# Kernel tuning notes

Hardware: AMD Instinct MI355X
Metric: run time of the kernel (lower is better)

Reference implementation:

```python
import jax, jax.numpy as jnp
import numpy as np

N = 50000
E = 1600000
D_IN = 128
HID = 128
EPS = 1e-5
NEG_SLOPE = 0.2


def setup_inputs() -> dict:
    key = jax.random.key(0)
    ks = jax.random.split(key, 16)
    s = 1.0 / np.sqrt(D_IN)
    inp = {
        'x': jax.random.normal(ks[0], (N, D_IN), dtype=jnp.float32),
        'edge_index': jax.random.randint(ks[1], (2, E), 0, N, dtype=jnp.int64),
        # layer 0 params
        'W0': jax.random.normal(ks[2], (D_IN, HID), dtype=jnp.float32) * s,
        'att_src0': jax.random.normal(ks[3], (HID,), dtype=jnp.float32) * s,
        'att_dst0': jax.random.normal(ks[4], (HID,), dtype=jnp.float32) * s,
        'bias0': jnp.zeros((HID,), dtype=jnp.float32),
        'gamma0': jnp.ones((HID,), dtype=jnp.float32),
        'beta0': jnp.zeros((HID,), dtype=jnp.float32),
        # layer 1 params
        'W1': jax.random.normal(ks[5], (HID, HID), dtype=jnp.float32) * s,
        'att_src1': jax.random.normal(ks[6], (HID,), dtype=jnp.float32) * s,
        'att_dst1': jax.random.normal(ks[7], (HID,), dtype=jnp.float32) * s,
        'bias1': jnp.zeros((HID,), dtype=jnp.float32),
        'gamma1': jnp.ones((HID,), dtype=jnp.float32),
        'beta1': jnp.zeros((HID,), dtype=jnp.float32),
    }
    return inp


def _gat_conv(x, W, a_src, a_dst, bias, src, dst, n_nodes):
    h = x @ W                                   # [N, HID]
    alpha_src = h @ a_src                       # [N]
    alpha_dst = h @ a_dst                       # [N]
    e = jax.nn.leaky_relu(alpha_src[src] + alpha_dst[dst], NEG_SLOPE)  # [E']
    # numerically stable softmax over edges grouped by destination node
    m = jax.ops.segment_max(e, dst, num_segments=n_nodes)
    ex = jnp.exp(e - m[dst])
    denom = jax.ops.segment_sum(ex, dst, num_segments=n_nodes)
    alpha = ex / denom[dst]                     # [E']
    out = jax.ops.segment_sum(h[src] * alpha[:, None], dst, num_segments=n_nodes)
    return out + bias


def _batch_norm(x, gamma, beta):
    mean = jnp.mean(x, axis=0)
    var = jnp.mean(jnp.square(x - mean), axis=0)  # biased variance (torch BN normalization)
    return gamma * (x - mean) * jax.lax.rsqrt(var + EPS) + beta


def reference(x, edge_index, W0, att_src0, att_dst0, bias0, gamma0, beta0,
              W1, att_src1, att_dst1, bias1, gamma1, beta1):
    n = x.shape[0]
    loops = jnp.arange(n, dtype=edge_index.dtype)
    src = jnp.concatenate([edge_index[0], loops])
    dst = jnp.concatenate([edge_index[1], loops])

    h = _gat_conv(x, W0, att_src0, att_dst0, bias0, src, dst, n)
    h = _batch_norm(h, gamma0, beta0)
    h = jax.nn.relu(h)
    # dropout: identity in eval mode

    h = _gat_conv(h, W1, att_src1, att_dst1, bias1, src, dst, n)
    h = _batch_norm(h, gamma1, beta1)
    h = jax.nn.relu(h)  # last_activation=True
    return h
```

## Files before the change

kernel.cpp:

```cpp
#include <hip/hip_runtime.h>
#include <math.h>

#define HID 128
#define PAD 96
#define NB 196
#define CAP 10240
#define CHUNK 4096
#define AGG_BLOCKS 2048
#define NEG_SLOPE 0.2f
#define EPS 1e-5f

static __device__ __forceinline__ unsigned bf16_rne(float x) {
    unsigned u = __float_as_uint(x);
    return (u + 0x7fffu + ((u >> 16) & 1u)) >> 16;
}
static __device__ __forceinline__ unsigned pack_bf16(float lo, float hi) {
    return bf16_rne(lo) | (bf16_rne(hi) << 16);
}

template <bool BN>
__global__ __launch_bounds__(256) void gemm_alpha(
    const float* __restrict__ X, const float* __restrict__ W,
    const float* __restrict__ a_src, const float* __restrict__ a_dst,
    const float* __restrict__ coef,
    unsigned* __restrict__ Hb, float* __restrict__ asrc, float* __restrict__ adst,
    int N)
{
    __shared__ float Ws[HID * HID];
    int tid = threadIdx.x;
#pragma unroll
    for (int i = 0; i < 16; ++i) {
        int idx = tid * 4 + i * 1024;
        *(float4*)&Ws[idx] = *(const float4*)&W[idx];
    }
    __syncthreads();

    int tx = tid & 15, ty = tid >> 4;
    int row0 = blockIdx.x * 128 + ty * 8;
    int c0 = tx * 8;

    const float* xr[8];
    bool valid[8];
#pragma unroll
    for (int r = 0; r < 8; ++r) {
        int row = row0 + r;
        valid[r] = (row < N);
        xr[r] = X + (size_t)(valid[r] ? row : 0) * HID;
    }

    float acc[8][8];
#pragma unroll
    for (int r = 0; r < 8; ++r)
#pragma unroll
        for (int c = 0; c < 8; ++c) acc[r][c] = 0.f;

    for (int kb = 0; kb < HID / 4; ++kb) {
        float4 sc4, sh4;
        if (BN) {
            sc4 = *(const float4*)&coef[kb * 4];
            sh4 = *(const float4*)&coef[HID + kb * 4];
        }
        float4 xv[8];
#pragma unroll
        for (int r = 0; r < 8; ++r) {
            xv[r] = *(const float4*)(xr[r] + kb * 4);
            if (BN) {
                xv[r].x = fmaxf(fmaf(xv[r].x, sc4.x, sh4.x), 0.f);
                xv[r].y = fmaxf(fmaf(xv[r].y, sc4.y, sh4.y), 0.f);
                xv[r].z = fmaxf(fmaf(xv[r].z, sc4.z, sh4.z), 0.f);
                xv[r].w = fmaxf(fmaf(xv[r].w, sc4.w, sh4.w), 0.f);
            }
        }
#pragma unroll
        for (int kk = 0; kk < 4; ++kk) {
            float4 w0 = *(const float4*)&Ws[(kb * 4 + kk) * HID + c0];
            float4 w1 = *(const float4*)&Ws[(kb * 4 + kk) * HID + c0 + 4];
#pragma unroll
            for (int r = 0; r < 8; ++r) {
                float xk = (&xv[r].x)[kk];
                acc[r][0] = fmaf(xk, w0.x, acc[r][0]);
                acc[r][1] = fmaf(xk, w0.y, acc[r][1]);
                acc[r][2] = fmaf(xk, w0.z, acc[r][2]);
                acc[r][3] = fmaf(xk, w0.w, acc[r][3]);
                acc[r][4] = fmaf(xk, w1.x, acc[r][4]);
                acc[r][5] = fmaf(xk, w1.y, acc[r][5]);
                acc[r][6] = fmaf(xk, w1.z, acc[r][6]);
                acc[r][7] = fmaf(xk, w1.w, acc[r][7]);
            }
        }
    }

    float4 asv0 = *(const float4*)&a_src[c0];
    float4 asv1 = *(const float4*)&a_src[c0 + 4];
    float4 adv0 = *(const float4*)&a_dst[c0];
    float4 adv1 = *(const float4*)&a_dst[c0 + 4];

#pragma unroll
    for (int r = 0; r < 8; ++r) {
        float s = acc[r][0] * asv0.x + acc[r][1] * asv0.y + acc[r][2] * asv0.z +
                  acc[r][3] * asv0.w + acc[r][4] * asv1.x + acc[r][5] * asv1.y +
                  acc[r][6] * asv1.z + acc[r][7] * asv1.w;
        float d = acc[r][0] * adv0.x + acc[r][1] * adv0.y + acc[r][2] * adv0.z +
                  acc[r][3] * adv0.w + acc[r][4] * adv1.x + acc[r][5] * adv1.y +
                  acc[r][6] * adv1.z + acc[r][7] * adv1.w;
#pragma unroll
        for (int o = 1; o < 16; o <<= 1) {
            s += __shfl_xor(s, o);
            d += __shfl_xor(d, o);
        }
        if (tx == 0 && valid[r]) { asrc[row0 + r] = s; adst[row0 + r] = d; }
        if (valid[r]) {
            uint4 st;
            st.x = pack_bf16(acc[r][0], acc[r][1]);
            st.y = pack_bf16(acc[r][2], acc[r][3]);
            st.z = pack_bf16(acc[r][4], acc[r][5]);
            st.w = pack_bf16(acc[r][6], acc[r][7]);
            *(uint4*)&Hb[(size_t)(row0 + r) * 64 + (c0 >> 1)] = st;
        }
    }
}

__global__ __launch_bounds__(256) void scatter_part(
    const int* __restrict__ ei, int* __restrict__ bcur,
    unsigned int* __restrict__ bbuf, int E)
{
    __shared__ int lcnt[NB], gbase[NB];
    int tid = threadIdx.x;
    int i0 = blockIdx.x * CHUNK;
    int i1 = i0 + CHUNK; if (i1 > E) i1 = E;
    if (tid < NB) lcnt[tid] = 0;
    __syncthreads();
    for (int i = i0 + tid; i < i1; i += 256)
        atomicAdd(&lcnt[ei[E + i] >> 8], 1);
    __syncthreads();
    if (tid < NB) {
        gbase[tid] = atomicAdd(&bcur[tid], lcnt[tid]);
        lcnt[tid] = 0;
    }
    __syncthreads();
    for (int i = i0 + tid; i < i1; i += 256) {
        int s = ei[i], d = ei[E + i];
        int b = d >> 8;
        int off = atomicAdd(&lcnt[b], 1);
        int pos = gbase[b] + off;
        if (pos < CAP)
            bbuf[(size_t)b * CAP + pos] = ((unsigned)s << 8) | (unsigned)(d & 255);
    }
}

__global__ __launch_bounds__(256) void ell_build(
    const unsigned int* __restrict__ bbuf, const int* __restrict__ bcur,
    int* __restrict__ cnt, int* __restrict__ ell, int N)
{
    __shared__ int stage[256 * PAD];
    __shared__ int scnt[256];
    int tid = threadIdx.x;
    int b = blockIdx.x;
    int base = b << 8;
    int nodes = N - base; if (nodes > 256) nodes = 256;

    for (int i = tid; i < nodes; i += 256) {
        stage[i * PAD] = base + i;
        scnt[i] = 1;
    }
    __syncthreads();

    int nb = bcur[b]; if (nb > CAP) nb = CAP;
    const unsigned int* buf = bbuf + (size_t)b * CAP;
    for (int j = tid; j < nb; j += 256) {
        unsigned int v = buf[j];
        int dl = (int)(v & 255u);
        int s = (int)(v >> 8);
        int p = atomicAdd(&scnt[dl], 1);
        if (p < PAD) stage[dl * PAD + p] = s;
    }
    __syncthreads();

    int total = nodes * PAD;
    int* dst = ell + (size_t)base * PAD;
    for (int idx = tid * 4; idx < total; idx += 1024)
        *(int4*)&dst[idx] = *(const int4*)&stage[idx];
    for (int i = tid; i < nodes; i += 256)
        cnt[base + i] = scnt[i];
}

__global__ __launch_bounds__(256) void gat_aggregate(
    const unsigned* __restrict__ Hb, const float* __restrict__ asrc,
    const float* __restrict__ adst, const int* __restrict__ cnt,
    const int* __restrict__ ell, const float* __restrict__ bias,
    float* __restrict__ OUT, float* __restrict__ stat, int N)
{
    __shared__ float sbuf[4][HID], qbuf[4][HID];
    int tid = threadIdx.x, wave = tid >> 6, lane = tid & 63;
    int c0 = 2 * lane;
    float b0 = bias[c0], b1 = bias[c0 + 1];
    float ssum0 = 0.f, ssum1 = 0.f, sq0 = 0.f, sq1 = 0.f;

    for (int n = blockIdx.x * 4 + wave; n < N; n += AGG_BLOCKS * 4) {
        int nn = __builtin_amdgcn_readfirstlane(n);
        int deg = cnt[nn];
        if (deg > PAD) deg = PAD;
        const int* row = ell + (size_t)nn * PAD;
        float adn = adst[nn];

        float acc0 = 0.f, acc1 = 0.f, den = 0.f;
#define EDGE(SI) { int si = (SI);                                   \
        float v = asrc[si] + adn;                                   \
        v = v > 0.f ? v : NEG_SLOPE * v;                            \
        float w = __expf(v);                                        \
        den += w;                                                   \
        unsigned hv = Hb[(size_t)si * 64 + lane];                   \
        acc0 = fmaf(w, __uint_as_float(hv << 16), acc0);            \
        acc1 = fmaf(w, __uint_as_float(hv & 0xffff0000u), acc1); }
        int j = 0;
        for (; j + 4 <= deg; j += 4) {
            int4 s4 = *(const int4*)&row[j];
            EDGE(s4.x) EDGE(s4.y) EDGE(s4.z) EDGE(s4.w)
        }
        for (; j < deg; ++j) EDGE(row[j])
#undef EDGE
        float inv = 1.f / den;
        float o0 = fmaf(acc0, inv, b0);
        float o1 = fmaf(acc1, inv, b1);
        *(float2*)&OUT[(size_t)nn * HID + c0] = make_float2(o0, o1);
        ssum0 += o0; ssum1 += o1;
        sq0 = fmaf(o0, o0, sq0); sq1 = fmaf(o1, o1, sq1);
    }

    sbuf[wave][c0] = ssum0; sbuf[wave][c0 + 1] = ssum1;
    qbuf[wave][c0] = sq0;   qbuf[wave][c0 + 1] = sq1;
    __syncthreads();
    if (tid < HID) {
        float t = sbuf[0][tid] + sbuf[1][tid] + sbuf[2][tid] + sbuf[3][tid];
        atomicAdd(&stat[tid], t);
    } else {
        int c = tid - HID;
        float t = qbuf[0][c] + qbuf[1][c] + qbuf[2][c] + qbuf[3][c];
        atomicAdd(&stat[HID + c], t);
    }
}

__global__ void bn_coef(const float* __restrict__ stat, const float* __restrict__ gamma,
                        const float* __restrict__ beta, float* __restrict__ coef,
                        float invN)
{
    int c = threadIdx.x;
    float mean = stat[c] * invN;
    float var = stat[HID + c] * invN - mean * mean;
    float s = gamma[c] * rsqrtf(var + EPS);
    coef[c] = s;
    coef[HID + c] = beta[c] - mean * s;
}

__global__ __launch_bounds__(256) void bn_apply(
    float* __restrict__ X, const float* __restrict__ coef, int N)
{
    int tid = threadIdx.x, lane = tid & 63, wave = tid >> 6;
    int c0 = 2 * lane;
    float s0 = coef[c0], s1 = coef[c0 + 1];
    float h0 = coef[HID + c0], h1 = coef[HID + c0 + 1];
    for (int r = blockIdx.x * 4 + wave; r < N; r += gridDim.x * 4) {
        float2 v = *(float2*)&X[(size_t)r * HID + c0];
        float y0 = fmaxf(fmaf(v.x, s0, h0), 0.f);
        float y1 = fmaxf(fmaf(v.y, s1, h1), 0.f);
        *(float2*)&X[(size_t)r * HID + c0] = make_float2(y0, y1);
    }
}

extern "C" void kernel_launch(void* const* d_in, const int* in_sizes, int n_in,
                              void* d_out, int out_size, void* d_ws, size_t ws_size,
                              hipStream_t stream)
{
    const float* x        = (const float*)d_in[0];
    const int*   ei       = (const int*)d_in[1];
    const float* W0       = (const float*)d_in[2];
    const float* att_src0 = (const float*)d_in[3];
    const float* att_dst0 = (const float*)d_in[4];
    const float* bias0    = (const float*)d_in[5];
    const float* gamma0   = (const float*)d_in[6];
    const float* beta0    = (const float*)d_in[7];
    const float* W1       = (const float*)d_in[8];
    const float* att_src1 = (const float*)d_in[9];
    const float* att_dst1 = (const float*)d_in[10];
    const float* bias1    = (const float*)d_in[11];
    const float* gamma1   = (const float*)d_in[12];
    const float* beta1    = (const float*)d_in[13];

    const int N = in_sizes[0] / HID;
    const int E = in_sizes[1] / 2;
    float* out = (float*)d_out;

    char* wsbase = (char*)d_ws;
    size_t off = 0;
    auto alloc = [&](size_t bytes) -> void* {
        void* p = wsbase + off;
        off += (bytes + 255) & ~(size_t)255;
        return p;
    };
    unsigned*     Hb    = (unsigned*)alloc((size_t)N * HID * 2);
    float*        asrc  = (float*)alloc((size_t)N * 4);
    float*        adst  = (float*)alloc((size_t)N * 4);
    int*          cnt   = (int*)  alloc((size_t)N * 4);
    int*          ell   = (int*)  alloc((size_t)N * PAD * 4);
    unsigned int* bbuf  = (unsigned int*)alloc((size_t)NB * CAP * 4);
    int*          bcur  = (int*)  alloc(NB * 4);
    float*        stats = (float*)alloc(4 * HID * 4);
    float*        coef0 = (float*)alloc(2 * HID * 4);
    float*        coef1 = (float*)alloc(2 * HID * 4);
    float* stat0 = stats;
    float* stat1 = stats + 2 * HID;

    const int gemm_blocks = (N + 127) / 128;
    const int part_blocks = (E + CHUNK - 1) / CHUNK;
    const int build_blocks = (N + 255) / 256;
    const float invN = 1.0f / (float)N;

    (void)hipMemsetAsync(bcur, 0, NB * 4, stream);
    (void)hipMemsetAsync(stats, 0, 4 * HID * 4, stream);

    scatter_part<<<part_blocks, 256, 0, stream>>>(ei, bcur, bbuf, E);
    ell_build<<<build_blocks, 256, 0, stream>>>(bbuf, bcur, cnt, ell, N);

    gemm_alpha<false><<<gemm_blocks, 256, 0, stream>>>(
        x, W0, att_src0, att_dst0, nullptr, Hb, asrc, adst, N);
    gat_aggregate<<<AGG_BLOCKS, 256, 0, stream>>>(
        Hb, asrc, adst, cnt, ell, bias0, out, stat0, N);
    bn_coef<<<1, HID, 0, stream>>>(stat0, gamma0, beta0, coef0, invN);

    gemm_alpha<true><<<gemm_blocks, 256, 0, stream>>>(
        out, W1, att_src1, att_dst1, coef0, Hb, asrc, adst, N);
    gat_aggregate<<<AGG_BLOCKS, 256, 0, stream>>>(
        Hb, asrc, adst, cnt, ell, bias1, out, stat1, N);
    bn_coef<<<1, HID, 0, stream>>>(stat1, gamma1, beta1, coef1, invN);
    bn_apply<<<2048, 256, 0, stream>>>(out, coef1, N);
}
```

Measured before the change: 325.7 us.

## Use bf16 MFMA for feature GEMM and half-wave-per-node aggregation

Replaces the FP32 register-tiled GEMM with bf16 MFMA 16x16x32 instructions, reading a transposed bf16 copy of each weight matrix that a small kernel builds at the start. The aggregation kernel now gives each half-wave one node and each lane four channels, loading edges in groups of eight with masking, and zero-fills the ELL staging so the padded slots are safe to read. This is meant to cut GEMM compute time and raise memory-level parallelism in the gather. In exchange, the input activations are also rounded to bf16, which adds precision loss, and the gather does some wasted work on padded edges.

New measurement: 338.3 us. 3.9% more time.

```diff
diff --git a/kernel.cpp b/kernel.cpp
--- a/kernel.cpp
+++ b/kernel.cpp
@@ -10,112 +10,114 @@
 #define NEG_SLOPE 0.2f
 #define EPS 1e-5f
 
+typedef __attribute__((ext_vector_type(8))) short short8;
+typedef __attribute__((ext_vector_type(4))) float floatx4;
+
 static __device__ __forceinline__ unsigned bf16_rne(float x) {
     unsigned u = __float_as_uint(x);
     return (u + 0x7fffu + ((u >> 16) & 1u)) >> 16;
 }
-static __device__ __forceinline__ unsigned pack_bf16(float lo, float hi) {
-    return bf16_rne(lo) | (bf16_rne(hi) << 16);
+static __device__ __forceinline__ float bf16lo_f(unsigned u) { return __uint_as_float(u << 16); }
+static __device__ __forceinline__ float bf16hi_f(unsigned u) { return __uint_as_float(u & 0xffff0000u); }
+
+__global__ void wt_build(const float* __restrict__ W, unsigned short* __restrict__ Wt) {
+    int t = threadIdx.x;
+    for (int task = t; task < 2048; task += 256) {
+        int c = task & 127, k0 = (task >> 7) * 8;
+        unsigned v[8];
+#pragma unroll
+        for (int j = 0; j < 8; ++j) v[j] = bf16_rne(W[(k0 + j) * HID + c]);
+        uint4 st;
+        st.x = v[0] | (v[1] << 16);
+        st.y = v[2] | (v[3] << 16);
+        st.z = v[4] | (v[5] << 16);
+        st.w = v[6] | (v[7] << 16);
+        *(uint4*)&Wt[c * HID + k0] = st;
+    }
 }
 
 template <bool BN>
-__global__ __launch_bounds__(256) void gemm_alpha(
-    const float* __restrict__ X, const float* __restrict__ W,
+__global__ __launch_bounds__(256) void gemm_mfma(
+    const float* __restrict__ X, const unsigned short* __restrict__ Wt,
     const float* __restrict__ a_src, const float* __restrict__ a_dst,
     const float* __restrict__ coef,
-    unsigned* __restrict__ Hb, float* __restrict__ asrc, float* __restrict__ adst,
+    unsigned short* __restrict__ Hb, float* __restrict__ asrc, float* __restrict__ adst,
     int N)
 {
-    __shared__ float Ws[HID * HID];
     int tid = threadIdx.x;
-#pragma unroll
-    for (int i = 0; i < 16; ++i) {
-        int idx = tid * 4 + i * 1024;
-        *(float4*)&Ws[idx] = *(const float4*)&W[idx];
-    }
-    __syncthreads();
-
-    int tx = tid & 15, ty = tid >> 4;
-    int row0 = blockIdx.x * 128 + ty * 8;
-    int c0 = tx * 8;
-
-    const float* xr[8];
-    bool valid[8];
-#pragma unroll
-    for (int r = 0; r < 8; ++r) {
-        int row = row0 + r;
-        valid[r] = (row < N);
-        xr[r] = X + (size_t)(valid[r] ? row : 0) * HID;
-    }
-
-    float acc[8][8];
-#pragma unroll
-    for (int r = 0; r < 8; ++r)
-#pragma unroll
-        for (int c = 0; c < 8; ++c) acc[r][c] = 0.f;
-
-    for (int kb = 0; kb < HID / 4; ++kb) {
-        float4 sc4, sh4;
+    int wv = tid >> 6, lane = tid & 63;
+    int g = lane >> 4, c = lane & 15;
+    int r0w = blockIdx.x * 64 + wv * 16;
+    int arow = r0w + c;
+    bool avalid = arow < N;
+    const float* xr = X + (size_t)(avalid ? arow : 0) * HID;
+
+    floatx4 acc[8];
+#pragma unroll
+    for (int i = 0; i < 8; ++i) acc[i] = (floatx4)0.f;
+
+#pragma unroll
+    for (int kc = 0; kc < 4; ++kc) {
+        int k0 = kc * 32 + g * 8;
+        float xv[8];
+        float4 x0 = *(const float4*)&xr[k0];
+        float4 x1 = *(const float4*)&xr[k0 + 4];
+        xv[0] = x0.x; xv[1] = x0.y; xv[2] = x0.z; xv[3] = x0.w;
+        xv[4] = x1.x; xv[5] = x1.y; xv[6] = x1.z; xv[7] = x1.w;
         if (BN) {
-            sc4 = *(const float4*)&coef[kb * 4];
-            sh4 = *(const float4*)&coef[HID + kb * 4];
-        }
-        float4 xv[8];
-#pragma unroll
-        for (int r = 0; r < 8; ++r) {
-            xv[r] = *(const float4*)(xr[r] + kb * 4);
-            if (BN) {
-                xv[r].x = fmaxf(fmaf(xv[r].x, sc4.x, sh4.x), 0.f);
-                xv[r].y = fmaxf(fmaf(xv[r].y, sc4.y, sh4.y), 0.f);
-                xv[r].z = fmaxf(fmaf(xv[r].z, sc4.z, sh4.z), 0.f);
-                xv[r].w = fmaxf(fmaf(xv[r].w, sc4.w, sh4.w), 0.f);
-            }
-        }
-#pragma unroll
-        for (int kk = 0; kk < 4; ++kk) {
-            float4 w0 = *(const float4*)&Ws[(kb * 4 + kk) * HID + c0];
-            float4 w1 = *(const float4*)&Ws[(kb * 4 + kk) * HID + c0 + 4];
-#pragma unroll
-            for (int r = 0; r < 8; ++r) {
-                float xk = (&xv[r].x)[kk];
-                acc[r][0] = fmaf(xk, w0.x, acc[r][0]);
-                acc[r][1] = fmaf(xk, w0.y, acc[r][1]);
-                acc[r][2] = fmaf(xk, w0.z, acc[r][2]);
-                acc[r][3] = fmaf(xk, w0.w, acc[r][3]);
-                acc[r][4] = fmaf(xk, w1.x, acc[r][4]);
-                acc[r][5] = fmaf(xk, w1.y, acc[r][5]);
-                acc[r][6] = fmaf(xk, w1.z, acc[r][6]);
-                acc[r][7] = fmaf(xk, w1.w, acc[r][7]);
-            }
-        }
-    }
-
-    float4 asv0 = *(const float4*)&a_src[c0];
-    float4 asv1 = *(const float4*)&a_src[c0 + 4];
-    float4 adv0 = *(const float4*)&a_dst[c0];
-    float4 adv1 = *(const float4*)&a_dst[c0 + 4];
-
-#pragma unroll
-    for (int r = 0; r < 8; ++r) {
-        float s = acc[r][0] * asv0.x + acc[r][1] * asv0.y + acc[r][2] * asv0.z +
-                  acc[r][3] * asv0.w + acc[r][4] * asv1.x + acc[r][5] * asv1.y +
-                  acc[r][6] * asv1.z + acc[r][7] * asv1.w;
-        float d = acc[r][0] * adv0.x + acc[r][1] * adv0.y + acc[r][2] * adv0.z +
-                  acc[r][3] * adv0.w + acc[r][4] * adv1.x + acc[r][5] * adv1.y +
-                  acc[r][6] * adv1.z + acc[r][7] * adv1.w;
+            float4 s0 = *(const float4*)&coef[k0];
+            float4 s1 = *(const float4*)&coef[k0 + 4];
+            float4 h0 = *(const float4*)&coef[HID + k0];
+            float4 h1 = *(const float4*)&coef[HID + k0 + 4];
+            xv[0] = fmaxf(fmaf(xv[0], s0.x, h0.x), 0.f);
+            xv[1] = fmaxf(fmaf(xv[1], s0.y, h0.y), 0.f);
+            xv[2] = fmaxf(fmaf(xv[2], s0.z, h0.z), 0.f);
+            xv[3] = fmaxf(fmaf(xv[3], s0.w, h0.w), 0.f);
+            xv[4] = fmaxf(fmaf(xv[4], s1.x, h1.x), 0.f);
+            xv[5] = fmaxf(fmaf(xv[5], s1.y, h1.y), 0.f);
+            xv[6] = fmaxf(fmaf(xv[6], s1.z, h1.z), 0.f);
+            xv[7] = fmaxf(fmaf(xv[7], s1.w, h1.w), 0.f);
+        }
+        short8 af;
+#pragma unroll
+        for (int j = 0; j < 8; ++j) af[j] = avalid ? (short)bf16_rne(xv[j]) : (short)0;
+
+#pragma unroll
+        for (int nt = 0; nt < 8; ++nt) {
+            short8 bf = *(const short8*)&Wt[(nt * 16 + c) * HID + k0];
+            acc[nt] = __builtin_amdgcn_mfma_f32_16x16x32_bf16(af, bf, acc[nt], 0, 0, 0);
+        }
+    }
+
+    float as_c[8], ad_c[8];
+#pragma unroll
+    for (int nt = 0; nt < 8; ++nt) {
+        as_c[nt] = a_src[nt * 16 + c];
+        ad_c[nt] = a_dst[nt * 16 + c];
+    }
+#pragma unroll
+    for (int reg = 0; reg < 4; ++reg) {
+        float s = 0.f, d = 0.f;
+#pragma unroll
+        for (int nt = 0; nt < 8; ++nt) {
+            s = fmaf(acc[nt][reg], as_c[nt], s);
+            d = fmaf(acc[nt][reg], ad_c[nt], d);
+        }
 #pragma unroll
         for (int o = 1; o < 16; o <<= 1) {
             s += __shfl_xor(s, o);
             d += __shfl_xor(d, o);
         }
-        if (tx == 0 && valid[r]) { asrc[row0 + r] = s; adst[row0 + r] = d; }
-        if (valid[r]) {
-            uint4 st;
-            st.x = pack_bf16(acc[r][0], acc[r][1]);
-            st.y = pack_bf16(acc[r][2], acc[r][3]);
-            st.z = pack_bf16(acc[r][4], acc[r][5]);
-            st.w = pack_bf16(acc[r][6], acc[r][7]);
-            *(uint4*)&Hb[(size_t)(row0 + r) * 64 + (c0 >> 1)] = st;
+        int crow = r0w + g * 4 + reg;
+        if (c == 0 && crow < N) { asrc[crow] = s; adst[crow] = d; }
+    }
+#pragma unroll
+    for (int reg = 0; reg < 4; ++reg) {
+        int crow = r0w + g * 4 + reg;
+        if (crow < N) {
+#pragma unroll
+            for (int nt = 0; nt < 8; ++nt)
+                Hb[(size_t)crow * HID + nt * 16 + c] = (unsigned short)bf16_rne(acc[nt][reg]);
         }
     }
 }
@@ -159,6 +161,10 @@
     int base = b << 8;
     int nodes = N - base; if (nodes > 256) nodes = 256;
 
+    int4 z4; z4.x = z4.y = z4.z = z4.w = 0;
+    for (int idx = tid * 4; idx < 256 * PAD; idx += 1024)
+        *(int4*)&stage[idx] = z4;
+    __syncthreads();
     for (int i = tid; i < nodes; i += 256) {
         stage[i * PAD] = base + i;
         scnt[i] = 1;
@@ -185,58 +191,72 @@
 }
 
 __global__ __launch_bounds__(256) void gat_aggregate(
-    const unsigned* __restrict__ Hb, const float* __restrict__ asrc,
+    const unsigned short* __restrict__ Hb, const float* __restrict__ asrc,
     const float* __restrict__ adst, const int* __restrict__ cnt,
     const int* __restrict__ ell, const float* __restrict__ bias,
     float* __restrict__ OUT, float* __restrict__ stat, int N)
 {
     __shared__ float sbuf[4][HID], qbuf[4][HID];
-    int tid = threadIdx.x, wave = tid >> 6, lane = tid & 63;
-    int c0 = 2 * lane;
-    float b0 = bias[c0], b1 = bias[c0 + 1];
-    float ssum0 = 0.f, ssum1 = 0.f, sq0 = 0.f, sq1 = 0.f;
-
-    for (int n = blockIdx.x * 4 + wave; n < N; n += AGG_BLOCKS * 4) {
-        int nn = __builtin_amdgcn_readfirstlane(n);
-        int deg = cnt[nn];
-        if (deg > PAD) deg = PAD;
-        const int* row = ell + (size_t)nn * PAD;
-        float adn = adst[nn];
-
-        float acc0 = 0.f, acc1 = 0.f, den = 0.f;
-#define EDGE(SI) { int si = (SI);                                   \
-        float v = asrc[si] + adn;                                   \
-        v = v > 0.f ? v : NEG_SLOPE * v;                            \
-        float w = __expf(v);                                        \
-        den += w;                                                   \
-        unsigned hv = Hb[(size_t)si * 64 + lane];                   \
-        acc0 = fmaf(w, __uint_as_float(hv << 16), acc0);            \
-        acc1 = fmaf(w, __uint_as_float(hv & 0xffff0000u), acc1); }
-        int j = 0;
-        for (; j + 4 <= deg; j += 4) {
-            int4 s4 = *(const int4*)&row[j];
-            EDGE(s4.x) EDGE(s4.y) EDGE(s4.z) EDGE(s4.w)
-        }
-        for (; j < deg; ++j) EDGE(row[j])
-#undef EDGE
+    int tid = threadIdx.x, wv = tid >> 6, lane = tid & 63;
+    int half = lane >> 5, li = lane & 31;
+    int c0 = 4 * li;
+    float4 b4 = *(const float4*)&bias[c0];
+    float s0 = 0.f, s1 = 0.f, s2 = 0.f, s3 = 0.f;
+    float q0 = 0.f, q1 = 0.f, q2 = 0.f, q3 = 0.f;
+
+    for (int n = blockIdx.x * 8 + wv * 2 + half; n < N; n += AGG_BLOCKS * 8) {
+        int deg = cnt[n]; if (deg > PAD) deg = PAD;
+        const int* row = ell + (size_t)n * PAD;
+        float adn = adst[n];
+        float a0 = 0.f, a1 = 0.f, a2 = 0.f, a3 = 0.f, den = 0.f;
+
+        for (int j = 0; j < deg; j += 8) {
+            int4 sA = *(const int4*)&row[j];
+            int4 sB = *(const int4*)&row[j + 4];
+#define EDG(SI, JOFF) { int si = (SI);                                \
+            float v = asrc[si] + adn;                                 \
+            v = fmaxf(v, 0.f) + NEG_SLOPE * fminf(v, 0.f);            \
+            float w = ((j + JOFF) < deg) ? __expf(v) : 0.f;           \
+            den += w;                                                 \
+            uint2 hv = *(const uint2*)&Hb[(size_t)si * HID + c0];     \
+            a0 = fmaf(w, bf16lo_f(hv.x), a0);                         \
+            a1 = fmaf(w, bf16hi_f(hv.x), a1);                         \
+            a2 = fmaf(w, bf16lo_f(hv.y), a2);                         \
+            a3 = fmaf(w, bf16hi_f(hv.y), a3); }
+            EDG(sA.x, 0) EDG(sA.y, 1) EDG(sA.z, 2) EDG(sA.w, 3)
+            EDG(sB.x, 4) EDG(sB.y, 5) EDG(sB.z, 6) EDG(sB.w, 7)
+#undef EDG
+        }
         float inv = 1.f / den;
-        float o0 = fmaf(acc0, inv, b0);
-        float o1 = fmaf(acc1, inv, b1);
-        *(float2*)&OUT[(size_t)nn * HID + c0] = make_float2(o0, o1);
-        ssum0 += o0; ssum1 += o1;
-        sq0 = fmaf(o0, o0, sq0); sq1 = fmaf(o1, o1, sq1);
-    }
-
-    sbuf[wave][c0] = ssum0; sbuf[wave][c0 + 1] = ssum1;
-    qbuf[wave][c0] = sq0;   qbuf[wave][c0 + 1] = sq1;
+        float4 o;
+        o.x = fmaf(a0, inv, b4.x);
+        o.y = fmaf(a1, inv, b4.y);
+        o.z = fmaf(a2, inv, b4.z);
+        o.w = fmaf(a3, inv, b4.w);
+        *(float4*)&OUT[(size_t)n * HID + c0] = o;
+        s0 += o.x; s1 += o.y; s2 += o.z; s3 += o.w;
+        q0 = fmaf(o.x, o.x, q0); q1 = fmaf(o.y, o.y, q1);
+        q2 = fmaf(o.z, o.z, q2); q3 = fmaf(o.w, o.w, q3);
+    }
+
+    s0 += __shfl_xor(s0, 32); s1 += __shfl_xor(s1, 32);
+    s2 += __shfl_xor(s2, 32); s3 += __shfl_xor(s3, 32);
+    q0 += __shfl_xor(q0, 32); q1 += __shfl_xor(q1, 32);
+    q2 += __shfl_xor(q2, 32); q3 += __shfl_xor(q3, 32);
+    if (half == 0) {
+        sbuf[wv][c0] = s0; sbuf[wv][c0 + 1] = s1;
+        sbuf[wv][c0 + 2] = s2; sbuf[wv][c0 + 3] = s3;
+        qbuf[wv][c0] = q0; qbuf[wv][c0 + 1] = q1;
+        qbuf[wv][c0 + 2] = q2; qbuf[wv][c0 + 3] = q3;
+    }
     __syncthreads();
     if (tid < HID) {
         float t = sbuf[0][tid] + sbuf[1][tid] + sbuf[2][tid] + sbuf[3][tid];
         atomicAdd(&stat[tid], t);
     } else {
-        int c = tid - HID;
-        float t = qbuf[0][c] + qbuf[1][c] + qbuf[2][c] + qbuf[3][c];
-        atomicAdd(&stat[HID + c], t);
+        int cc = tid - HID;
+        float t = qbuf[0][cc] + qbuf[1][cc] + qbuf[2][cc] + qbuf[3][cc];
+        atomicAdd(&stat[HID + cc], t);
     }
 }
 
@@ -255,11 +275,11 @@
 __global__ __launch_bounds__(256) void bn_apply(
     float* __restrict__ X, const float* __restrict__ coef, int N)
 {
-    int tid = threadIdx.x, lane = tid & 63, wave = tid >> 6;
+    int tid = threadIdx.x, lane = tid & 63, wv = tid >> 6;
     int c0 = 2 * lane;
     float s0 = coef[c0], s1 = coef[c0 + 1];
     float h0 = coef[HID + c0], h1 = coef[HID + c0 + 1];
-    for (int r = blockIdx.x * 4 + wave; r < N; r += gridDim.x * 4) {
+    for (int r = blockIdx.x * 4 + wv; r < N; r += gridDim.x * 4) {
         float2 v = *(float2*)&X[(size_t)r * HID + c0];
         float y0 = fmaxf(fmaf(v.x, s0, h0), 0.f);
         float y1 = fmaxf(fmaf(v.y, s1, h1), 0.f);
@@ -297,38 +317,42 @@
         off += (bytes + 255) & ~(size_t)255;
         return p;
     };
-    unsigned*     Hb    = (unsigned*)alloc((size_t)N * HID * 2);
-    float*        asrc  = (float*)alloc((size_t)N * 4);
-    float*        adst  = (float*)alloc((size_t)N * 4);
-    int*          cnt   = (int*)  alloc((size_t)N * 4);
-    int*          ell   = (int*)  alloc((size_t)N * PAD * 4);
-    unsigned int* bbuf  = (unsigned int*)alloc((size_t)NB * CAP * 4);
-    int*          bcur  = (int*)  alloc(NB * 4);
-    float*        stats = (float*)alloc(4 * HID * 4);
-    float*        coef0 = (float*)alloc(2 * HID * 4);
-    float*        coef1 = (float*)alloc(2 * HID * 4);
+    unsigned short* Hb   = (unsigned short*)alloc((size_t)N * HID * 2);
+    float*          asrc = (float*)alloc((size_t)N * 4);
+    float*          adst = (float*)alloc((size_t)N * 4);
+    int*            cnt  = (int*)  alloc((size_t)N * 4);
+    int*            ell  = (int*)  alloc((size_t)N * PAD * 4);
+    unsigned int*   bbuf = (unsigned int*)alloc((size_t)NB * CAP * 4);
+    int*            bcur = (int*)  alloc(NB * 4);
+    float*          stats = (float*)alloc(4 * HID * 4);
+    float*          coef0 = (float*)alloc(2 * HID * 4);
+    float*          coef1 = (float*)alloc(2 * HID * 4);
+    unsigned short* Wt0  = (unsigned short*)alloc(HID * HID * 2);
+    unsigned short* Wt1  = (unsigned short*)alloc(HID * HID * 2);
     float* stat0 = stats;
     float* stat1 = stats + 2 * HID;
 
-    const int gemm_blocks = (N + 127) / 128;
-    const int part_blocks = (E + CHUNK - 1) / CHUNK;
+    const int gemm_blocks  = (N + 63) / 64;
+    const int part_blocks  = (E + CHUNK - 1) / CHUNK;
     const int build_blocks = (N + 255) / 256;
     const float invN = 1.0f / (float)N;
 
     (void)hipMemsetAsync(bcur, 0, NB * 4, stream);
     (void)hipMemsetAsync(stats, 0, 4 * HID * 4, stream);
 
+    wt_build<<<1, 256, 0, stream>>>(W0, Wt0);
+    wt_build<<<1, 256, 0, stream>>>(W1, Wt1);
     scatter_part<<<part_blocks, 256, 0, stream>>>(ei, bcur, bbuf, E);
     ell_build<<<build_blocks, 256, 0, stream>>>(bbuf, bcur, cnt, ell, N);
 
-    gemm_alpha<false><<<gemm_blocks, 256, 0, stream>>>(
-        x, W0, att_src0, att_dst0, nullptr, Hb, asrc, adst, N);
+    gemm_mfma<false><<<gemm_blocks, 256, 0, stream>>>(
+        x, Wt0, att_src0, att_dst0, nullptr, Hb, asrc, adst, N);
     gat_aggregate<<<AGG_BLOCKS, 256, 0, stream>>>(
         Hb, asrc, adst, cnt, ell, bias0, out, stat0, N);
     bn_coef<<<1, HID, 0, stream>>>(stat0, gamma0, beta0, coef0, invN);
 
-    gemm_alpha<true><<<gemm_blocks, 256, 0, stream>>>(
-        out, W1, att_src1, att_dst1, coef0, Hb, asrc, adst, N);
+    gemm_mfma<true><<<gemm_blocks, 256, 0, stream>>>(
+        out, Wt1, att_src1, att_dst1, coef0, Hb, asrc, adst, N);
     gat_aggregate<<<AGG_BLOCKS, 256, 0, stream>>>(
         Hb, asrc, adst, cnt, ell, bias1, out, stat1, N);
     bn_coef<<<1, HID, 0, stream>>>(stat1, gamma1, beta1, coef1, invN);
```
